# Performance work log

Measured on AMD Instinct MI355X. Metric: run time of the kernel, lower is better.

The kernel has to match this reference:

```python
import jax, jax.numpy as jnp
import numpy as np

N = 25000
E = 400000
HIDDEN = 512
NH = 8
DH = HIDDEN // NH


def setup_inputs() -> dict:
    key = jax.random.key(0)
    ks = jax.random.split(key, 10)
    s = 1.0 / np.sqrt(HIDDEN)
    return {
        "h": jax.random.normal(ks[0], (N, HIDDEN), dtype=jnp.float32),
        "Wq": jax.random.normal(ks[1], (HIDDEN, HIDDEN), dtype=jnp.float32) * s,
        "bq": jnp.zeros((HIDDEN,), dtype=jnp.float32),
        "Wk": jax.random.normal(ks[2], (HIDDEN, HIDDEN), dtype=jnp.float32) * s,
        "bk": jnp.zeros((HIDDEN,), dtype=jnp.float32),
        "Wo": jax.random.normal(ks[3], (HIDDEN, HIDDEN), dtype=jnp.float32) * s,
        "bo": jnp.zeros((HIDDEN,), dtype=jnp.float32),
        "rows": jax.random.randint(ks[4], (E,), 0, N, dtype=jnp.int32),
        "cols": jax.random.randint(ks[5], (E,), 0, N, dtype=jnp.int32),
    }


def reference(h, Wq, bq, Wk, bk, Wo, bo, rows, cols):
    # Projections; reshape (N, dh, nh) exactly as the source does.
    q = (h @ Wq + bq).reshape(N, DH, NH)
    k = (h @ Wk + bk).reshape(N, DH, NH)
    v = k  # source bug kept faithfully: v = linear_k(h)

    # SDDMM: per-edge, per-head dot product (no 1/sqrt(dh) scaling in source).
    scores = jnp.einsum("edh,edh->eh", q[rows], k[cols])  # [E, NH]

    # Row-wise (source-node) segment softmax per head.
    m = jax.ops.segment_max(scores, rows, num_segments=N)       # [N, NH]
    ex = jnp.exp(scores - m[rows])                              # [E, NH]
    denom = jax.ops.segment_sum(ex, rows, num_segments=N)      # [N, NH]
    attn = ex / denom[rows]                                     # [E, NH]

    # SpMM: out[i] = sum_{j in nbr(i)} attn[ij] * v[j]
    msgs = attn[:, None, :] * v[cols]                           # [E, DH, NH]
    out = jax.ops.segment_sum(msgs, rows, num_segments=N)      # [N, DH, NH]

    return out.reshape(N, HIDDEN) @ Wo + bo
```

## Files before the change

kernel.cpp:

```cpp
#include <hip/hip_runtime.h>
#include <math.h>

typedef unsigned short u16;
typedef unsigned int u32;
typedef __attribute__((ext_vector_type(8))) _Float16 half8;
typedef __attribute__((ext_vector_type(2))) _Float16 half2v;
typedef __attribute__((ext_vector_type(8))) u16 ushort8;
typedef __attribute__((ext_vector_type(4))) float f32x4;

__device__ __forceinline__ u16 f2h(float f) {
    union { u16 u; _Float16 h; } c; c.h = (_Float16)f; return c.u;
}

#if __has_builtin(__builtin_amdgcn_fdot2)
#define FDOT2(a, b, c) __builtin_amdgcn_fdot2((a), (b), (c), false)
#else
#define FDOT2(a, b, c) fmaf((float)(a)[0], (float)(b)[0], \
                        fmaf((float)(a)[1], (float)(b)[1], (c)))
#endif

__device__ __forceinline__ void gload16(void* lds, const void* g) {
    __builtin_amdgcn_global_load_lds(
        (const __attribute__((address_space(1))) u32*)g,
        (__attribute__((address_space(3))) u32*)lds,
        16, 0, 0);
}

template <int OUTMODE>
__device__ __forceinline__ void gemm_body(
    const u16* A, const u16* Bt, const float* bias, void* Cout, int Mout,
    int m0, int n0, u16* As0, u16* As1, u16* Bs0, u16* Bs1)
{
    const int tid  = threadIdx.x;
    const int wave = tid >> 6;
    const int lane = tid & 63;
    const int wr = (wave >> 1) * 64;
    const int wc = (wave & 1) * 64;

    f32x4 acc[4][4];
#pragma unroll
    for (int i = 0; i < 4; ++i)
#pragma unroll
        for (int j = 0; j < 4; ++j) acc[i][j] = (f32x4){0.f, 0.f, 0.f, 0.f};

    const int srow  = lane >> 2;
    const int scolG = ((lane & 3) ^ ((srow >> 1) & 3)) * 8;
    const size_t gOffA = (size_t)(m0 + wave * 32 + srow) * 512 + scolG;
    const size_t gOffB = (size_t)(n0 + wave * 32 + srow) * 512 + scolG;
    const int lOff = wave * 1024 + srow * 32 + (lane & 3) * 8;

    const int fR = ((lane & 15) >> 1) & 3;
    const int paOff = (wr + (lane & 15)) * 32 + ((lane >> 4) ^ fR) * 8;
    const int pbOff = (wc + (lane & 15)) * 32 + ((lane >> 4) ^ fR) * 8;

    auto STAGE = [&](u16* sa, u16* sb, int ko) {
        gload16(sa + lOff,       A  + gOffA + ko);
        gload16(sa + lOff + 512, A  + gOffA + ko + 16 * 512);
        gload16(sb + lOff,       Bt + gOffB + ko);
        gload16(sb + lOff + 512, Bt + gOffB + ko + 16 * 512);
    };
    auto COMPUTE = [&](const u16* sa, const u16* sb) {
        half8 af[4], bf[4];
#pragma unroll
        for (int i = 0; i < 4; ++i) af[i] = *(const half8*)(sa + paOff + i * 512);
#pragma unroll
        for (int j = 0; j < 4; ++j) bf[j] = *(const half8*)(sb + pbOff + j * 512);
#pragma unroll
        for (int i = 0; i < 4; ++i)
#pragma unroll
            for (int j = 0; j < 4; ++j)
                acc[i][j] = __builtin_amdgcn_mfma_f32_16x16x32_f16(
                    af[i], bf[j], acc[i][j], 0, 0, 0);
    };

    STAGE(As0, Bs0, 0);
    __syncthreads();
#pragma unroll
    for (int kt = 0; kt < 16; kt += 2) {
        STAGE(As1, Bs1, (kt + 1) * 32);
        COMPUTE(As0, Bs0);
        __syncthreads();
        if (kt + 2 < 16) STAGE(As0, Bs0, (kt + 2) * 32);
        COMPUTE(As1, Bs1);
        __syncthreads();
    }

    const int ccol  = n0 + wc + (lane & 15);
    const int crow0 = m0 + wr + (lane >> 4) * 4;
#pragma unroll
    for (int j = 0; j < 4; ++j) {
        const float b = bias[ccol + j * 16];
#pragma unroll
        for (int i = 0; i < 4; ++i) {
#pragma unroll
            for (int r = 0; r < 4; ++r) {
                int row = crow0 + i * 16 + r;
                if (row < Mout) {
                    float v = acc[i][j][r] + b;
                    size_t off = (size_t)row * 512 + ccol + j * 16;
                    if (OUTMODE == 0) ((float*)Cout)[off] = v;
                    else              ((u16*)Cout)[off] = f2h(v);
                }
            }
        }
    }
}

__global__ __launch_bounds__(256) void gemm_qk(
    const u16* __restrict__ hh, const u16* __restrict__ Wqt,
    const u16* __restrict__ Wkt, const float* __restrict__ bqp,
    const float* __restrict__ bkp, u16* __restrict__ Qh,
    u16* __restrict__ Kb, int nPad)
{
    __shared__ __align__(16) u16 As0[4096], As1[4096], Bs0[4096], Bs1[4096];
    const u16* Bt = blockIdx.z ? Wkt : Wqt;
    const float* bias = blockIdx.z ? bkp : bqp;
    u16* out = blockIdx.z ? Kb : Qh;
    gemm_body<1>(hh, Bt, bias, out, nPad, blockIdx.x * 128, blockIdx.y * 128,
                 As0, As1, Bs0, Bs1);
}

__global__ __launch_bounds__(256) void gemm_wo(
    const u16* __restrict__ A, const u16* __restrict__ Wot,
    const float* __restrict__ bo, float* __restrict__ C, int Mout)
{
    __shared__ __align__(16) u16 As0[4096], As1[4096], Bs0[4096], Bs1[4096];
    gemm_body<0>(A, Wot, bo, C, Mout, blockIdx.x * 128, blockIdx.y * 128,
                 As0, As1, Bs0, Bs1);
}

__global__ __launch_bounds__(256) void prep(
    const float* __restrict__ h, u16* __restrict__ hh, int nN,
    const int* __restrict__ rows, int* __restrict__ deg, int E,
    const float* __restrict__ Wq, const float* __restrict__ Wk,
    const float* __restrict__ Wo, const float* __restrict__ bq,
    const float* __restrict__ bk,
    u16* __restrict__ Wqt, u16* __restrict__ Wkt, u16* __restrict__ Wot,
    float* __restrict__ bqp, float* __restrict__ bkp,
    int nbH, int nbE)
{
    __shared__ float T[64][65];
    const int tid = threadIdx.x;
    const int b = blockIdx.x;

    if (b < nbH) {
        int t = b * 256 + tid;
        size_t e = (size_t)t * 8;
        int row = (int)(e >> 9);
        ushort8 o;
        if (row < nN) {
            f32x4 a = *(const f32x4*)(h + e);
            f32x4 bb = *(const f32x4*)(h + e + 4);
            float x[8] = {a.x, a.y, a.z, a.w, bb.x, bb.y, bb.z, bb.w};
#pragma unroll
            for (int i = 0; i < 8; ++i) o[i] = f2h(x[i]);
        } else {
            o = (ushort8){0,0,0,0,0,0,0,0};
        }
        *(ushort8*)(hh + e) = o;
        return;
    }
    if (b < nbH + nbE) {
        int i = (b - nbH) * 256 + tid;
        if (i < E) atomicAdd(&deg[rows[i]], 1);
        return;
    }
    int rem = b - nbH - nbE;
    const int z = rem >> 6;
    const int X = (rem & 7) * 64;
    const int Y = ((rem >> 3) & 7) * 64;

    const int r4 = tid >> 4;
    const int c4 = (tid & 15) * 4;
    if (z < 2) {
        const float* W = z ? Wk : Wq;
#pragma unroll
        for (int rr = 0; rr < 64; rr += 16) {
            f32x4 v = *(const f32x4*)(W + (size_t)(X + rr + r4) * 512 + Y + c4);
            T[rr + r4][c4 + 0] = v.x; T[rr + r4][c4 + 1] = v.y;
            T[rr + r4][c4 + 2] = v.z; T[rr + r4][c4 + 3] = v.w;
        }
    } else {
#pragma unroll
        for (int rr = 0; rr < 64; rr += 16) {
            int p2 = (rr + r4) * 8 + (X >> 6);
            f32x4 v = *(const f32x4*)(Wo + (size_t)p2 * 512 + Y + c4);
            T[rr + r4][c4 + 0] = v.x; T[rr + r4][c4 + 1] = v.y;
            T[rr + r4][c4 + 2] = v.z; T[rr + r4][c4 + 3] = v.w;
        }
    }
    __syncthreads();

    const int cc = tid >> 2;
    const int ks = (tid & 3) * 16;
    const int pc = Y + cc;
    const int ro = (z < 2) ? ((pc & 7) * 64 + (pc >> 3)) : pc;
    ushort8 h0, h1;
#pragma unroll
    for (int t = 0; t < 8; ++t) {
        h0[t] = f2h(T[ks + t][cc]);
        h1[t] = f2h(T[ks + 8 + t][cc]);
    }
    size_t o = (size_t)ro * 512 + X + ks;
    if (z == 0) {
        *(ushort8*)(Wqt + o) = h0; *(ushort8*)(Wqt + o + 8) = h1;
    } else if (z == 1) {
        *(ushort8*)(Wkt + o) = h0; *(ushort8*)(Wkt + o + 8) = h1;
    } else {
        *(ushort8*)(Wot + o) = h0; *(ushort8*)(Wot + o + 8) = h1;
        if (rem == 128) {
            for (int bi = tid; bi < 512; bi += 256) {
                int pp = (bi & 63) * 8 + (bi >> 6);
                bqp[bi] = bq[pp];
                bkp[bi] = bk[pp];
            }
        }
    }
}

#define SCAN_CHUNK 2048

__global__ __launch_bounds__(256) void scan_partial(
    const int* __restrict__ deg, int* __restrict__ bsum, int n)
{
    int base = blockIdx.x * SCAN_CHUNK;
    int t = threadIdx.x;
    int s = 0;
    for (int i = t; i < SCAN_CHUNK; i += 256) {
        int g = base + i;
        s += (g < n) ? deg[g] : 0;
    }
#pragma unroll
    for (int off = 1; off < 64; off <<= 1) s += __shfl_xor(s, off, 64);
    __shared__ int ws[4];
    if ((t & 63) == 0) ws[t >> 6] = s;
    __syncthreads();
    if (t == 0) bsum[blockIdx.x] = ws[0] + ws[1] + ws[2] + ws[3];
}

__global__ __launch_bounds__(256) void scan_final(
    const int* __restrict__ deg, const int* __restrict__ bsum,
    int* __restrict__ rowptr, int* __restrict__ cursor, int n, int nb)
{
    int boff = 0, total = 0;
    for (int i = 0; i < nb; ++i) {
        int v = bsum[i];
        if (i < (int)blockIdx.x) boff += v;
        total += v;
    }
    int t = threadIdx.x;
    int base = blockIdx.x * SCAN_CHUNK + t * 8;
    int v[8];
    int s = 0;
#pragma unroll
    for (int i = 0; i < 8; ++i) {
        int g = base + i;
        v[i] = (g < n) ? deg[g] : 0;
        s += v[i];
    }
    int lane = t & 63, w = t >> 6;
    int inc = s;
#pragma unroll
    for (int off = 1; off < 64; off <<= 1) {
        int x = __shfl_up(inc, off, 64);
        if (lane >= off) inc += x;
    }
    __shared__ int wsum[4];
    if (lane == 63) wsum[w] = inc;
    __syncthreads();
    int excl = boff + inc - s;
    for (int i = 0; i < w; ++i) excl += wsum[i];
#pragma unroll
    for (int i = 0; i < 8; ++i) {
        int g = base + i;
        if (g < n) { rowptr[g] = excl; cursor[g] = excl; }
        excl += v[i];
    }
    if (blockIdx.x == 0 && t == 0) rowptr[n] = total;
}

__global__ void scatter_kernel(const int* __restrict__ rows, const int* __restrict__ cols,
                               int* __restrict__ cursor, int* __restrict__ colc, int E)
{
    int i = blockIdx.x * 256 + threadIdx.x;
    if (i < E) {
        int pos = atomicAdd(&cursor[rows[i]], 1);
        colc[pos] = cols[i];
    }
}

__global__ __launch_bounds__(256) void node_agg(
    const u16* __restrict__ Qh, const u16* __restrict__ Kb,
    const int* __restrict__ rowptr, const int* __restrict__ colc,
    u16* __restrict__ aggb, int nN)
{
    int node = blockIdx.x * 4 + (threadIdx.x >> 6);
    int lane = threadIdx.x & 63;
    if (node >= nN) return;
    size_t base = (size_t)node * 512 + lane * 8;

    half8 qv = __builtin_nontemporal_load((const half8*)(Qh + base));
    half2v q2[4];
#pragma unroll
    for (int i = 0; i < 4; ++i) q2[i] = (half2v){qv[2 * i], qv[2 * i + 1]};

    int start = rowptr[node];
    int deg   = rowptr[node + 1] - start;
    const int* cp = colc + start;
    const size_t loff = (size_t)lane * 8;

    float m = -__builtin_inff();
    float den = 0.f;
    half2v acc2[4];
#pragma unroll
    for (int i = 0; i < 4; ++i) acc2[i] = (half2v){(_Float16)0.f, (_Float16)0.f};

    if (deg > 0) {
        const int dl = deg - 1;
        half8 k0 = *(const half8*)(Kb + (size_t)cp[0] * 512 + loff);
        half8 k1 = *(const half8*)(Kb + (size_t)cp[1 < dl ? 1 : dl] * 512 + loff);
        half8 k2 = *(const half8*)(Kb + (size_t)cp[2 < dl ? 2 : dl] * 512 + loff);
        half8 k3 = *(const half8*)(Kb + (size_t)cp[3 < dl ? 3 : dl] * 512 + loff);
        for (int j = 0; j < deg; j += 4) {
            int i4 = j + 4 < dl ? j + 4 : dl;
            int i5 = j + 5 < dl ? j + 5 : dl;
            int i6 = j + 6 < dl ? j + 6 : dl;
            int i7 = j + 7 < dl ? j + 7 : dl;
            half8 n0 = *(const half8*)(Kb + (size_t)cp[i4] * 512 + loff);
            half8 n1 = *(const half8*)(Kb + (size_t)cp[i5] * 512 + loff);
            half8 n2 = *(const half8*)(Kb + (size_t)cp[i6] * 512 + loff);
            half8 n3 = *(const half8*)(Kb + (size_t)cp[i7] * 512 + loff);

            float p0 = 0.f, p1 = 0.f, p2 = 0.f, p3 = 0.f;
#pragma unroll
            for (int i = 0; i < 4; ++i) {
                half2v a = q2[i];
                half2v b0 = (half2v){k0[2 * i], k0[2 * i + 1]};
                half2v b1 = (half2v){k1[2 * i], k1[2 * i + 1]};
                half2v b2 = (half2v){k2[2 * i], k2[2 * i + 1]};
                half2v b3 = (half2v){k3[2 * i], k3[2 * i + 1]};
                p0 = FDOT2(a, b0, p0);
                p1 = FDOT2(a, b1, p1);
                p2 = FDOT2(a, b2, p2);
                p3 = FDOT2(a, b3, p3);
            }
#pragma unroll
            for (int off = 1; off < 8; off <<= 1) {
                p0 += __shfl_xor(p0, off, 64);
                p1 += __shfl_xor(p1, off, 64);
                p2 += __shfl_xor(p2, off, 64);
                p3 += __shfl_xor(p3, off, 64);
            }

            float pm = fmaxf(fmaxf(p0, p1), fmaxf(p2, p3));
            if (__any(pm > m + 4.f)) {
                float mn = fmaxf(m, pm);
                float sc = __expf(m - mn);
                den *= sc;
                _Float16 sch = (_Float16)sc;
                half2v sc2 = {sch, sch};
#pragma unroll
                for (int i = 0; i < 4; ++i) acc2[i] *= sc2;
                m = mn;
            }
            float w0 = __expf(p0 - m);
            float w1 = (j + 1 < deg) ? __expf(p1 - m) : 0.f;
            float w2 = (j + 2 < deg) ? __expf(p2 - m) : 0.f;
            float w3 = (j + 3 < deg) ? __expf(p3 - m) : 0.f;
            den += (w0 + w1) + (w2 + w3);
            _Float16 h0 = (_Float16)w0, h1 = (_Float16)w1;
            _Float16 h2 = (_Float16)w2, h3 = (_Float16)w3;
            half2v w02 = {h0, h0}, w12 = {h1, h1}, w22 = {h2, h2}, w32 = {h3, h3};
#pragma unroll
            for (int i = 0; i < 4; ++i) {
                half2v b0 = (half2v){k0[2 * i], k0[2 * i + 1]};
                half2v b1 = (half2v){k1[2 * i], k1[2 * i + 1]};
                half2v b2 = (half2v){k2[2 * i], k2[2 * i + 1]};
                half2v b3 = (half2v){k3[2 * i], k3[2 * i + 1]};
                acc2[i] += w02 * b0;
                acc2[i] += w12 * b1;
                acc2[i] += w22 * b2;
                acc2[i] += w32 * b3;
            }
            k0 = n0; k1 = n1; k2 = n2; k3 = n3;
        }
    }

    float inv = (deg > 0) ? 1.f / den : 0.f;
    ushort8 o;
#pragma unroll
    for (int i = 0; i < 4; ++i) {
        o[2 * i]     = f2h((float)acc2[i][0] * inv);
        o[2 * i + 1] = f2h((float)acc2[i][1] * inv);
    }
    __builtin_nontemporal_store(o, (ushort8*)(aggb + base));
}

extern "C" void kernel_launch(void* const* d_in, const int* in_sizes, int n_in,
                              void* d_out, int out_size, void* d_ws, size_t ws_size,
                              hipStream_t stream)
{
    const float* h  = (const float*)d_in[0];
    const float* Wq = (const float*)d_in[1];
    const float* bq = (const float*)d_in[2];
    const float* Wk = (const float*)d_in[3];
    const float* bk = (const float*)d_in[4];
    const float* Wo = (const float*)d_in[5];
    const float* bo = (const float*)d_in[6];
    const int* rows = (const int*)d_in[7];
    const int* cols = (const int*)d_in[8];
    float* out = (float*)d_out;

    const int HID = 512;
    const int nN  = in_sizes[0] / HID;
    const int E   = in_sizes[7];
    const int nPad = (nN + 127) & ~127;
    const int nb = (nN + SCAN_CHUNK - 1) / SCAN_CHUNK;
    const int nbH = nPad * (HID / 8) / 256;
    const int nbE = (E + 255) / 256;

    char* w = (char*)d_ws;
    u16* Kb  = (u16*)w;  w += (size_t)nPad * HID * 2;
    u16* hh  = (u16*)w;  w += (size_t)nPad * HID * 2;
    u16* Qh  = (u16*)w;  w += (size_t)nPad * HID * 2;
    u16* Wqt = (u16*)w;  w += 512 * 512 * 2;
    u16* Wkt = (u16*)w;  w += 512 * 512 * 2;
    u16* Wot = (u16*)w;  w += 512 * 512 * 2;
    float* bqp = (float*)w;  w += 512 * 4;
    float* bkp = (float*)w;  w += 512 * 4;
    int* rowptr = (int*)w;   w += (size_t)(nN + 1) * 4;
    int* cursor = (int*)w;   w += (size_t)nN * 4;
    int* deg    = (int*)w;   w += (size_t)nN * 4;
    int* bsum   = (int*)w;   w += 64 * 4;
    int* colc   = (int*)w;

    (void)hipMemsetAsync(deg, 0, (size_t)nN * sizeof(int), stream);

    prep<<<nbH + nbE + 192, 256, 0, stream>>>(
        h, hh, nN, rows, deg, E, Wq, Wk, Wo, bq, bk,
        Wqt, Wkt, Wot, bqp, bkp, nbH, nbE);

    scan_partial<<<nb, 256, 0, stream>>>(deg, bsum, nN);
    scan_final<<<nb, 256, 0, stream>>>(deg, bsum, rowptr, cursor, nN, nb);
    scatter_kernel<<<(E + 255) / 256, 256, 0, stream>>>(rows, cols, cursor, colc, E);

    gemm_qk<<<dim3(nPad / 128, 4, 2), 256, 0, stream>>>(
        hh, Wqt, Wkt, bqp, bkp, Qh, Kb, nPad);

    node_agg<<<(nN + 3) / 4, 256, 0, stream>>>(Qh, Kb, rowptr, colc, hh, nN);

    gemm_wo<<<dim3(nPad / 128, 4), 256, 0, stream>>>(hh, Wot, bo, out, nN);
}
```

Measured before the change: 234.8 us.

## Deepen GEMM LDS pipeline to four buffers with explicit vmcnt waits

Replaces the double-buffered K loop in the shared GEMM body with a four-slot ring that keeps two stages of global-to-LDS loads in flight. Each iteration uses a manual s_waitcnt vmcnt plus a single barrier instead of two __syncthreads, so the memory latency of the Q/K and Wo projections can overlap further with MFMA work. This doubles LDS use per block (64 KB), which may lower occupancy. It also relies on hand-counted outstanding-load numbers and reuses a ring slot with only one barrier per step, which is fragile.

```diff
diff --git a/kernel.cpp b/kernel.cpp
--- a/kernel.cpp
+++ b/kernel.cpp
@@ -29,7 +29,7 @@
 template <int OUTMODE>
 __device__ __forceinline__ void gemm_body(
     const u16* A, const u16* Bt, const float* bias, void* Cout, int Mout,
-    int m0, int n0, u16* As0, u16* As1, u16* Bs0, u16* Bs1)
+    int m0, int n0, u16* AsB, u16* BsB)
 {
     const int tid  = threadIdx.x;
     const int wave = tid >> 6;
@@ -53,13 +53,17 @@
     const int paOff = (wr + (lane & 15)) * 32 + ((lane >> 4) ^ fR) * 8;
     const int pbOff = (wc + (lane & 15)) * 32 + ((lane >> 4) ^ fR) * 8;
 
-    auto STAGE = [&](u16* sa, u16* sb, int ko) {
+    auto STAGE = [&](int buf, int ko) {
+        u16* sa = AsB + buf * 4096;
+        u16* sb = BsB + buf * 4096;
         gload16(sa + lOff,       A  + gOffA + ko);
         gload16(sa + lOff + 512, A  + gOffA + ko + 16 * 512);
         gload16(sb + lOff,       Bt + gOffB + ko);
         gload16(sb + lOff + 512, Bt + gOffB + ko + 16 * 512);
     };
-    auto COMPUTE = [&](const u16* sa, const u16* sb) {
+    auto COMPUTE = [&](int buf) {
+        const u16* sa = AsB + buf * 4096;
+        const u16* sb = BsB + buf * 4096;
         half8 af[4], bf[4];
 #pragma unroll
         for (int i = 0; i < 4; ++i) af[i] = *(const half8*)(sa + paOff + i * 512);
@@ -73,16 +77,16 @@
                     af[i], bf[j], acc[i][j], 0, 0, 0);
     };
 
-    STAGE(As0, Bs0, 0);
-    __syncthreads();
-#pragma unroll
-    for (int kt = 0; kt < 16; kt += 2) {
-        STAGE(As1, Bs1, (kt + 1) * 32);
-        COMPUTE(As0, Bs0);
-        __syncthreads();
-        if (kt + 2 < 16) STAGE(As0, Bs0, (kt + 2) * 32);
-        COMPUTE(As1, Bs1);
-        __syncthreads();
+    STAGE(0, 0);
+    STAGE(1, 32);
+#pragma unroll
+    for (int kt = 0; kt < 16; ++kt) {
+        if (kt + 2 < 16) STAGE((kt + 2) & 3, (kt + 2) * 32);
+        if (kt <= 13)      asm volatile("s_waitcnt vmcnt(8)" ::: "memory");
+        else if (kt == 14) asm volatile("s_waitcnt vmcnt(4)" ::: "memory");
+        else               asm volatile("s_waitcnt vmcnt(0)" ::: "memory");
+        __builtin_amdgcn_s_barrier();
+        COMPUTE(kt & 3);
     }
 
     const int ccol  = n0 + wc + (lane & 15);
@@ -112,21 +116,21 @@
     const float* __restrict__ bkp, u16* __restrict__ Qh,
     u16* __restrict__ Kb, int nPad)
 {
-    __shared__ __align__(16) u16 As0[4096], As1[4096], Bs0[4096], Bs1[4096];
+    __shared__ __align__(16) u16 AsB[4 * 4096], BsB[4 * 4096];
     const u16* Bt = blockIdx.z ? Wkt : Wqt;
     const float* bias = blockIdx.z ? bkp : bqp;
     u16* out = blockIdx.z ? Kb : Qh;
     gemm_body<1>(hh, Bt, bias, out, nPad, blockIdx.x * 128, blockIdx.y * 128,
-                 As0, As1, Bs0, Bs1);
+                 AsB, BsB);
 }
 
 __global__ __launch_bounds__(256) void gemm_wo(
     const u16* __restrict__ A, const u16* __restrict__ Wot,
     const float* __restrict__ bo, float* __restrict__ C, int Mout)
 {
-    __shared__ __align__(16) u16 As0[4096], As1[4096], Bs0[4096], Bs1[4096];
+    __shared__ __align__(16) u16 AsB[4 * 4096], BsB[4 * 4096];
     gemm_body<0>(A, Wot, bo, C, Mout, blockIdx.x * 128, blockIdx.y * 128,
-                 As0, As1, Bs0, Bs1);
+                 AsB, BsB);
 }
 
 __global__ __launch_bounds__(256) void prep(
```

Result: slower. 249.8 us (+6.4%).
